# Performance work log

Measured on AMD Instinct MI355X. Metric: run time of the kernel, lower is better.

The kernel has to match this reference:

```python
import jax, jax.numpy as jnp
import numpy as np

N = 512          # grid size
L = 1.0          # domain length
DX = L / (N - 1)
DT = 5e-7        # satisfies CFL: dt <= dx^2 / (4 * max_alpha)
NUM_STEPS = 500
MB = 256         # material_boundary[1]: columns [0, MB) are material 1


def setup_inputs() -> dict:
    key = jax.random.key(0)
    u0 = jax.random.normal(key, (N, N), dtype=jnp.float32)
    return {
        "u0": u0,
        "k1": jnp.ones((1,), jnp.float32) * 1.0,
        "k2": jnp.ones((1,), jnp.float32) * 1.5,
        "alpha1": jnp.ones((1,), jnp.float32) * 1.0,
        "alpha2": jnp.ones((1,), jnp.float32) * 0.8,
    }


def _step(T, alpha_col, k1, k2):
    # 5-point Laplacian on interior points
    dx2 = jnp.float32(DX * DX)
    lap = (T[:-2, 1:-1] + T[2:, 1:-1] + T[1:-1, :-2] + T[1:-1, 2:]
           - 4.0 * T[1:-1, 1:-1]) / dx2
    # explicit Euler update with per-column diffusivity alpha(j)
    Tn = T.at[1:-1, 1:-1].set(T[1:-1, 1:-1]
                              + jnp.float32(DT) * alpha_col[None, 1:-1] * lap)
    # interface continuity: column MB-1 set from flux-weighted neighbors of OLD T
    i = MB - 1
    Tn = Tn.at[:, i].set((k1 * T[:, i + 1] + k2 * T[:, i - 1]) / (k1 + k2))
    # Dirichlet zero boundaries
    Tn = Tn.at[0, :].set(0.0).at[-1, :].set(0.0)
    Tn = Tn.at[:, 0].set(0.0).at[:, -1].set(0.0)
    return Tn


def reference(u0, k1, k2, alpha1, alpha2):
    k1 = k1.reshape(())
    k2 = k2.reshape(())
    a1 = alpha1.reshape(())
    a2 = alpha2.reshape(())
    # material_map: columns [0, MB) -> alpha1, else alpha2 (rows identical)
    alpha_col = jnp.where(jnp.arange(N) < MB, a1, a2).astype(u0.dtype)

    def body(T, _):
        Tn = _step(T, alpha_col, k1, k2)
        return Tn, Tn

    # intermediate_steps[1:] == states after steps 1..num_steps-1
    _, outs = jax.lax.scan(body, u0, None, length=NUM_STEPS - 1)
    return outs  # [NUM_STEPS-1, N, N]
```

## Files before the change

kernel.cpp:

```cpp
#include <hip/hip_runtime.h>


#define GN 512
#define NSTEPS 499
#define MBND 256
#define INV_DX2 261121.0f
#define DT 5e-7f

#define TO 32
#define KMAX 16
#define LOAD 64
#define LSTR 68

__device__ __forceinline__ void lds_barrier() {
    asm volatile("s_waitcnt lgkmcnt(0)" ::: "memory");
    __builtin_amdgcn_s_barrier();
    asm volatile("" ::: "memory");
}

__device__ __forceinline__ float dpp_row_shr1(float x) {
    int v = __builtin_amdgcn_update_dpp(__float_as_int(x), __float_as_int(x),
                                        0x111, 0xf, 0xf, false);
    return __int_as_float(v);
}
__device__ __forceinline__ float dpp_row_shl1(float x) {
    int v = __builtin_amdgcn_update_dpp(__float_as_int(x), __float_as_int(x),
                                        0x101, 0xf, 0xf, false);
    return __int_as_float(v);
}

struct Prm {
    float Ac[4]; bool ifc[4]; bool bcl[4];
    float k1, k2, invk;
    bool aI, aC, aR;
};

__device__ __forceinline__ void srow(const float x[4], const float up[4],
                                     const float dn[4], float out[4],
                                     const Prm& p, bool brF)
{
    const float lf = dpp_row_shr1(x[3]);
    const float rg = dpp_row_shl1(x[0]);
    const float le[4] = {lf, x[0], x[1], x[2]};
    const float ri[4] = {x[1], x[2], x[3], rg};
    #pragma unroll
    for (int j = 0; j < 4; ++j) {
        float v = fmaf(p.Ac[j], fmaf(-4.0f, x[j], (up[j] + dn[j]) + (le[j] + ri[j])), x[j]);
        if (p.aI) v = p.ifc[j] ? (p.k1 * ri[j] + p.k2 * le[j]) * p.invk : v;
        if (p.aC) v = p.bcl[j] ? 0.0f : v;
        if (p.aR) v = brF ? 0.0f : v;
        out[j] = v;
    }
}

__device__ __forceinline__ void ld4(float d[4], const float* s) {
    const float4 v = *(const float4*)s;
    d[0] = v.x; d[1] = v.y; d[2] = v.z; d[3] = v.w;
}

template<int STEPS>
__global__ __launch_bounds__(1024) void heat_multi(
    const float* __restrict__ Tin, float* __restrict__ outBase,
    const float* __restrict__ k1p, const float* __restrict__ k2p,
    const float* __restrict__ a1p, const float* __restrict__ a2p)
{
    __shared__ float Sb[2][LOAD][LSTR];

    const int t  = threadIdx.x;
    const int bi = blockIdx.x >> 4;
    const int bj = blockIdx.x & 15;
    const int gi0 = bi * TO - KMAX;
    const int gj0 = bj * TO - KMAX;

    const int tx = t & 15, ty = t >> 4;
    const int lj0 = tx * 4;

    float C[4];
    {
        const bool innerB = (gi0 >= 0) && (gi0 + LOAD <= GN) &&
                            (gj0 >= 0) && (gj0 + LOAD <= GN);
        float4 v;
        if (innerB) {
            v = *(const float4*)&Tin[(size_t)(gi0 + ty) * GN + (gj0 + lj0)];
        } else {
            const int gi_ = gi0 + ty;
            float tmp[4];
            #pragma unroll
            for (int e = 0; e < 4; ++e) {
                const int gj_ = gj0 + lj0 + e;
                tmp[e] = ((unsigned)gi_ < GN && (unsigned)gj_ < GN)
                         ? Tin[(size_t)gi_ * GN + gj_] : 0.0f;
            }
            v = make_float4(tmp[0], tmp[1], tmp[2], tmp[3]);
        }
        *(float4*)&Sb[0][ty][lj0] = v;
        C[0] = v.x; C[1] = v.y; C[2] = v.z; C[3] = v.w;
    }

    const int rm1 = (ty >= 1) ? ty - 1 : 0;
    const int rm2 = (ty >= 2) ? ty - 2 : 0;
    const int rp1 = (ty <= LOAD - 2) ? ty + 1 : LOAD - 1;
    const int rp2 = (ty <= LOAD - 3) ? ty + 2 : LOAD - 1;

    Prm p;
    p.k1 = k1p[0]; p.k2 = k2p[0];
    const float a1 = a1p[0], a2 = a2p[0];
    p.invk = 1.0f / (p.k1 + p.k2);
    #pragma unroll
    for (int j = 0; j < 4; ++j) {
        const int gj_ = gj0 + lj0 + j;
        p.Ac[j]  = (DT * INV_DX2) * ((gj_ < MBND) ? a1 : a2);
        p.ifc[j] = (gj_ == MBND - 1);
        p.bcl[j] = (gj_ <= 0) || (gj_ >= GN - 1);
    }
    p.aI = (bj == 7) || (bj == 8);
    p.aC = (bj == 0) || (bj == 15);
    p.aR = (bi == 0) || (bi == 15);

    const int gi = gi0 + ty;
    const bool brM = (gi - 1 <= 0) || (gi - 1 >= GN - 1);
    const bool br0 = (gi     <= 0) || (gi     >= GN - 1);
    const bool brP = (gi + 1 <= 0) || (gi + 1 >= GN - 1);

    const bool own = (tx >= 4) && (tx < 12) && (ty >= KMAX) && (ty < KMAX + TO);
    float* dst = outBase + ((long)gi * GN + (gj0 + lj0));

    lds_barrier();

    constexpr int NG = STEPS / 2;
    #pragma unroll
    for (int g = 0; g < NG; ++g) {
        const float (*Rb)[LSTR] = Sb[g & 1];
        float (*Wb)[LSTR] = Sb[(g + 1) & 1];

        float A[4], B[4], D[4], E[4];
        ld4(A, &Rb[rm2][lj0]);
        ld4(B, &Rb[rm1][lj0]);
        ld4(D, &Rb[rp1][lj0]);
        ld4(E, &Rb[rp2][lj0]);

        float nB[4], nC[4], nD[4];
        srow(B, A, C, nB, p, brM);
        srow(C, B, D, nC, p, br0);
        srow(D, C, E, nD, p, brP);
        if (own) *(float4*)dst = make_float4(nC[0], nC[1], nC[2], nC[3]);
        dst += (long)GN * GN;

        float n2[4];
        srow(nC, nB, nD, n2, p, br0);
        if (own) *(float4*)dst = make_float4(n2[0], n2[1], n2[2], n2[3]);
        dst += (long)GN * GN;

        C[0] = n2[0]; C[1] = n2[1]; C[2] = n2[2]; C[3] = n2[3];

        if (g < NG - 1 || STEPS == 3) {
            *(float4*)&Wb[ty][lj0] = make_float4(C[0], C[1], C[2], C[3]);
            lds_barrier();
        }
    }

    if constexpr (STEPS == 3) {
        float B[4], D[4];
        ld4(B, &Sb[1][rm1][lj0]);
        ld4(D, &Sb[1][rp1][lj0]);
        float nC[4];
        srow(C, B, D, nC, p, br0);
        if (own) *(float4*)dst = make_float4(nC[0], nC[1], nC[2], nC[3]);
    }
}

extern "C" void kernel_launch(void* const* d_in, const int* in_sizes, int n_in,
                              void* d_out, int out_size, void* d_ws, size_t ws_size,
                              hipStream_t stream)
{
    const float* u0 = (const float*)d_in[0];
    const float* k1 = (const float*)d_in[1];
    const float* k2 = (const float*)d_in[2];
    const float* a1 = (const float*)d_in[3];
    const float* a2 = (const float*)d_in[4];
    float* out = (float*)d_out;

    const int pts = GN * GN;
    const float* src = u0;
    int done = 0;
    while (done < NSTEPS) {
        int steps = NSTEPS - done;
        if (steps > KMAX) steps = KMAX;
        float* ob = out + (size_t)done * pts;
        if (steps == KMAX)
            heat_multi<KMAX><<<256, 1024, 0, stream>>>(src, ob, k1, k2, a1, a2);
        else
            heat_multi<3><<<256, 1024, 0, stream>>>(src, ob, k1, k2, a1, a2);
        src = ob + (size_t)(steps - 1) * pts;
        done += steps;
    }
}
```

Measured before the change: 387.3 us.

## Replace block barriers with per-wave neighbor flags and single-step updates

Drops the workgroup-wide barrier that ran every two time steps, along with the redundant two-step halo recompute. Each wave now computes one step, writes its rows to the double-buffered LDS tile and publishes a per-wave step counter. Before the next step it spin-waits, with an acquire load and s_sleep, only until its two adjacent waves have reached the previous step. This aims to let waves drift out of lockstep and to cut extra halo arithmetic. The cost is one LDS exchange per step instead of one per two steps, plus the overhead and fairness risk of spin polling.

```diff
diff --git a/kernel.cpp b/kernel.cpp
--- a/kernel.cpp
+++ b/kernel.cpp
@@ -12,12 +12,6 @@
 #define LOAD 64
 #define LSTR 68
 
-__device__ __forceinline__ void lds_barrier() {
-    asm volatile("s_waitcnt lgkmcnt(0)" ::: "memory");
-    __builtin_amdgcn_s_barrier();
-    asm volatile("" ::: "memory");
-}
-
 __device__ __forceinline__ float dpp_row_shr1(float x) {
     int v = __builtin_amdgcn_update_dpp(__float_as_int(x), __float_as_int(x),
                                         0x111, 0xf, 0xf, false);
@@ -27,6 +21,12 @@
     int v = __builtin_amdgcn_update_dpp(__float_as_int(x), __float_as_int(x),
                                         0x101, 0xf, 0xf, false);
     return __int_as_float(v);
+}
+
+__device__ __forceinline__ void wait_ge(const int* f, int v) {
+    while (__atomic_load_n(f, __ATOMIC_ACQUIRE) < v) {
+        __builtin_amdgcn_s_sleep(1);
+    }
 }
 
 struct Prm {
@@ -65,6 +65,7 @@
     const float* __restrict__ a1p, const float* __restrict__ a2p)
 {
     __shared__ float Sb[2][LOAD][LSTR];
+    __shared__ int flagArr[16];
 
     const int t  = threadIdx.x;
     const int bi = blockIdx.x >> 4;
@@ -73,6 +74,7 @@
     const int gj0 = bj * TO - KMAX;
 
     const int tx = t & 15, ty = t >> 4;
+    const int w  = t >> 6;
     const int lj0 = tx * 4;
 
     float C[4];
@@ -96,11 +98,13 @@
         *(float4*)&Sb[0][ty][lj0] = v;
         C[0] = v.x; C[1] = v.y; C[2] = v.z; C[3] = v.w;
     }
+    if (t < 16) flagArr[t] = 0;
+    __syncthreads();
 
     const int rm1 = (ty >= 1) ? ty - 1 : 0;
-    const int rm2 = (ty >= 2) ? ty - 2 : 0;
     const int rp1 = (ty <= LOAD - 2) ? ty + 1 : LOAD - 1;
-    const int rp2 = (ty <= LOAD - 3) ? ty + 2 : LOAD - 1;
+    const int wm1 = (w == 0) ? 0 : w - 1;
+    const int wp1 = (w == 15) ? 15 : w + 1;
 
     Prm p;
     p.k1 = k1p[0]; p.k2 = k2p[0];
@@ -118,54 +122,35 @@
     p.aR = (bi == 0) || (bi == 15);
 
     const int gi = gi0 + ty;
-    const bool brM = (gi - 1 <= 0) || (gi - 1 >= GN - 1);
-    const bool br0 = (gi     <= 0) || (gi     >= GN - 1);
-    const bool brP = (gi + 1 <= 0) || (gi + 1 >= GN - 1);
+    const bool br0 = (gi <= 0) || (gi >= GN - 1);
 
     const bool own = (tx >= 4) && (tx < 12) && (ty >= KMAX) && (ty < KMAX + TO);
     float* dst = outBase + ((long)gi * GN + (gj0 + lj0));
 
-    lds_barrier();
-
-    constexpr int NG = STEPS / 2;
     #pragma unroll
-    for (int g = 0; g < NG; ++g) {
-        const float (*Rb)[LSTR] = Sb[g & 1];
-        float (*Wb)[LSTR] = Sb[(g + 1) & 1];
-
-        float A[4], B[4], D[4], E[4];
-        ld4(A, &Rb[rm2][lj0]);
+    for (int s = 1; s <= STEPS; ++s) {
+        if (s > 1) {
+            wait_ge(&flagArr[wm1], s - 1);
+            wait_ge(&flagArr[wp1], s - 1);
+        }
+        const float (*Rb)[LSTR] = Sb[(s - 1) & 1];
+        float B[4], D[4];
         ld4(B, &Rb[rm1][lj0]);
         ld4(D, &Rb[rp1][lj0]);
-        ld4(E, &Rb[rp2][lj0]);
 
-        float nB[4], nC[4], nD[4];
-        srow(B, A, C, nB, p, brM);
-        srow(C, B, D, nC, p, br0);
-        srow(D, C, E, nD, p, brP);
-        if (own) *(float4*)dst = make_float4(nC[0], nC[1], nC[2], nC[3]);
-        dst += (long)GN * GN;
-
-        float n2[4];
-        srow(nC, nB, nD, n2, p, br0);
-        if (own) *(float4*)dst = make_float4(n2[0], n2[1], n2[2], n2[3]);
-        dst += (long)GN * GN;
-
-        C[0] = n2[0]; C[1] = n2[1]; C[2] = n2[2]; C[3] = n2[3];
-
-        if (g < NG - 1 || STEPS == 3) {
-            *(float4*)&Wb[ty][lj0] = make_float4(C[0], C[1], C[2], C[3]);
-            lds_barrier();
-        }
-    }
-
-    if constexpr (STEPS == 3) {
-        float B[4], D[4];
-        ld4(B, &Sb[1][rm1][lj0]);
-        ld4(D, &Sb[1][rp1][lj0]);
         float nC[4];
         srow(C, B, D, nC, p, br0);
-        if (own) *(float4*)dst = make_float4(nC[0], nC[1], nC[2], nC[3]);
+
+        if (s < STEPS) {
+            float (*Wb)[LSTR] = Sb[s & 1];
+            *(float4*)&Wb[ty][lj0] = make_float4(nC[0], nC[1], nC[2], nC[3]);
+            if ((t & 63) == 0)
+                __atomic_store_n(&flagArr[w], s, __ATOMIC_RELEASE);
+        }
+        C[0] = nC[0]; C[1] = nC[1]; C[2] = nC[2]; C[3] = nC[3];
+
+        if (own) *(float4*)dst = make_float4(C[0], C[1], C[2], C[3]);
+        dst += (long)GN * GN;
     }
 }
 
```

New measurement: 319.6 us. 17.5% less time.

## Replace block-wide barriers with per-wave neighbor flags in LDS

Applied to the files above, without the earlier changes.

Each of the 16 waves now publishes its completed step number to a flag in shared memory. Before each two-step group, a wave waits only on its two neighboring waves' flags instead of hitting a full 1024-thread barrier. The intent is to let waves drift relative to each other and avoid the cost of whole-block synchronisation every two steps. In exchange it adds spin-waiting with s_sleep and relies on acquire/release ordering of LDS atomics, plus double-buffer reuse being safe under one-step skew between neighbors.

```diff
diff --git a/kernel.cpp b/kernel.cpp
--- a/kernel.cpp
+++ b/kernel.cpp
@@ -11,12 +11,7 @@
 #define KMAX 16
 #define LOAD 64
 #define LSTR 68
-
-__device__ __forceinline__ void lds_barrier() {
-    asm volatile("s_waitcnt lgkmcnt(0)" ::: "memory");
-    __builtin_amdgcn_s_barrier();
-    asm volatile("" ::: "memory");
-}
+#define PTS (GN * GN)
 
 __device__ __forceinline__ float dpp_row_shr1(float x) {
     int v = __builtin_amdgcn_update_dpp(__float_as_int(x), __float_as_int(x),
@@ -65,6 +60,7 @@
     const float* __restrict__ a1p, const float* __restrict__ a2p)
 {
     __shared__ float Sb[2][LOAD][LSTR];
+    __shared__ int fl[16];
 
     const int t  = threadIdx.x;
     const int bi = blockIdx.x >> 4;
@@ -73,6 +69,7 @@
     const int gj0 = bj * TO - KMAX;
 
     const int tx = t & 15, ty = t >> 4;
+    const int w  = t >> 6;
     const int lj0 = tx * 4;
 
     float C[4];
@@ -96,11 +93,15 @@
         *(float4*)&Sb[0][ty][lj0] = v;
         C[0] = v.x; C[1] = v.y; C[2] = v.z; C[3] = v.w;
     }
+    if (t < 16) fl[t] = 0;
+    __syncthreads();
 
     const int rm1 = (ty >= 1) ? ty - 1 : 0;
     const int rm2 = (ty >= 2) ? ty - 2 : 0;
     const int rp1 = (ty <= LOAD - 2) ? ty + 1 : LOAD - 1;
     const int rp2 = (ty <= LOAD - 3) ? ty + 2 : LOAD - 1;
+    const int wm = (w > 0) ? w - 1 : 0;
+    const int wp = (w < 15) ? w + 1 : 15;
 
     Prm p;
     p.k1 = k1p[0]; p.k2 = k2p[0];
@@ -125,14 +126,15 @@
     const bool own = (tx >= 4) && (tx < 12) && (ty >= KMAX) && (ty < KMAX + TO);
     float* dst = outBase + ((long)gi * GN + (gj0 + lj0));
 
-    lds_barrier();
-
     constexpr int NG = STEPS / 2;
     #pragma unroll
-    for (int g = 0; g < NG; ++g) {
-        const float (*Rb)[LSTR] = Sb[g & 1];
-        float (*Wb)[LSTR] = Sb[(g + 1) & 1];
-
+    for (int g = 1; g <= NG; ++g) {
+        if (g > 1) {
+            while (__atomic_load_n(&fl[wm], __ATOMIC_ACQUIRE) < g - 1 ||
+                   __atomic_load_n(&fl[wp], __ATOMIC_ACQUIRE) < g - 1)
+                __builtin_amdgcn_s_sleep(1);
+        }
+        const float (*Rb)[LSTR] = Sb[(g - 1) & 1];
         float A[4], B[4], D[4], E[4];
         ld4(A, &Rb[rm2][lj0]);
         ld4(B, &Rb[rm1][lj0]);
@@ -144,22 +146,27 @@
         srow(C, B, D, nC, p, br0);
         srow(D, C, E, nD, p, brP);
         if (own) *(float4*)dst = make_float4(nC[0], nC[1], nC[2], nC[3]);
-        dst += (long)GN * GN;
+        dst += (long)PTS;
 
         float n2[4];
         srow(nC, nB, nD, n2, p, br0);
         if (own) *(float4*)dst = make_float4(n2[0], n2[1], n2[2], n2[3]);
-        dst += (long)GN * GN;
+        dst += (long)PTS;
 
         C[0] = n2[0]; C[1] = n2[1]; C[2] = n2[2]; C[3] = n2[3];
 
-        if (g < NG - 1 || STEPS == 3) {
+        if (g < NG || STEPS == 3) {
+            float (*Wb)[LSTR] = Sb[g & 1];
             *(float4*)&Wb[ty][lj0] = make_float4(C[0], C[1], C[2], C[3]);
-            lds_barrier();
+            if ((t & 63) == 0)
+                __atomic_store_n(&fl[w], g, __ATOMIC_RELEASE);
         }
     }
 
     if constexpr (STEPS == 3) {
+        while (__atomic_load_n(&fl[wm], __ATOMIC_ACQUIRE) < 1 ||
+               __atomic_load_n(&fl[wp], __ATOMIC_ACQUIRE) < 1)
+            __builtin_amdgcn_s_sleep(1);
         float B[4], D[4];
         ld4(B, &Sb[1][rm1][lj0]);
         ld4(D, &Sb[1][rp1][lj0]);
@@ -180,18 +187,17 @@
     const float* a2 = (const float*)d_in[4];
     float* out = (float*)d_out;
 
-    const int pts = GN * GN;
     const float* src = u0;
     int done = 0;
     while (done < NSTEPS) {
         int steps = NSTEPS - done;
         if (steps > KMAX) steps = KMAX;
-        float* ob = out + (size_t)done * pts;
+        float* ob = out + (size_t)done * PTS;
         if (steps == KMAX)
             heat_multi<KMAX><<<256, 1024, 0, stream>>>(src, ob, k1, k2, a1, a2);
         else
             heat_multi<3><<<256, 1024, 0, stream>>>(src, ob, k1, k2, a1, a2);
-        src = ob + (size_t)(steps - 1) * pts;
+        src = ob + (size_t)(steps - 1) * PTS;
         done += steps;
     }
 }
```

After: 397.3 us. 2.6% more time.
